# Performance work log

Measured on AMD Instinct MI355X. Metric: run time of the kernel, lower is better.

The kernel has to match this reference:

```python
import jax, jax.numpy as jnp
import numpy as np

GROUPS = [1, 2, 2, 3]

def setup_inputs() -> dict:
    key = jax.random.key(0)
    ks = jax.random.split(key, 8)
    b, dim, h, w = 8, 256, 64, 64
    return {
        "x": jax.random.normal(ks[0], (b, dim, h, w), dtype=jnp.float32),
        "temperature": jnp.ones((4, 1, 1), dtype=jnp.float32),          # nn.Parameter(torch.ones(4,1,1))
        "w_qkv": jax.random.normal(ks[1], (3 * dim, dim)) * 0.02,        # Conv2d(dim,3dim,1,bias=False)
        "w_dw": jax.random.normal(ks[2], (3 * dim, 1, 3, 3)) * 0.1,      # depthwise 3x3, groups=3dim
        "w_proj": jax.random.normal(ks[3], (dim, dim)) * 0.02,           # Conv2d(dim,dim,1,bias=False)
        "w_gate": jax.random.normal(ks[4], (dim, dim)) * 0.02,           # Intra gatingConv (Conv1d k=1)
        "b_gate": jnp.zeros((dim,), dtype=jnp.float32),
        "w_down": jax.random.normal(ks[5], (dim // 2, dim)) * 0.02,      # Intra down
        "b_down": jnp.zeros((dim // 2,), dtype=jnp.float32),
        "w_up": jax.random.normal(ks[6], (dim, dim // 2)) * 0.02,        # Intra up
        "b_up": jnp.zeros((dim,), dtype=jnp.float32),
    }

def _l2norm(t):
    # torch F.normalize(dim=-1): x / max(||x||, 1e-12)
    return t / jnp.maximum(jnp.linalg.norm(t, axis=-1, keepdims=True), 1e-12)

def reference(x, temperature, w_qkv, w_dw, w_proj, w_gate, b_gate, w_down, b_down, w_up, b_up):
    b, c, h, w = x.shape
    L = h * w
    # qkv = dwconv3x3(conv1x1(x))
    qkv = jnp.einsum('bchw,oc->bohw', x, w_qkv)
    qkv = jax.lax.conv_general_dilated(qkv, w_dw, (1, 1), ((1, 1), (1, 1)),
                                       feature_group_count=3 * c,
                                       dimension_numbers=('NCHW', 'OIHW', 'NCHW'))
    q, k, v = jnp.split(qkv, 3, axis=1)
    q = q.reshape(b, c, L); k = k.reshape(b, c, L); v = v.reshape(b, c, L)
    # ReGroup: sort channels by mean activation (descending), split per ratio
    order = jnp.argsort(-q.mean(axis=2).mean(axis=0))
    qs, ks_, vs = q[:, order], k[:, order], v[:, order]
    total = sum(GROUPS)
    sizes = [int(r / total * c) for r in GROUPS]
    sizes[-1] += c - sum(sizes)
    outs, caches = [], []
    start = 0
    for i, g in enumerate(sizes):
        qg = qs[:, start:start + g]; kg = ks_[:, start:start + g]; vg = vs[:, start:start + g]
        start += g
        qn = _l2norm(qg); kn = _l2norm(kg)
        attn = jax.nn.softmax(jnp.einsum('bcl,bdl->bcd', qn, kn) * temperature[i], axis=-1)  # (b,Cg,Cg)
        caches.append(jax.lax.stop_gradient(qn + kn))  # q.detach()+k.detach()
        outs.append(jnp.einsum('bcd,bdl->bcl', attn, vg))
    # CalculateCurrentLayerCache: mean over L, channel-tile to c, bilinear 1x1->sxs == broadcast
    s = int(L ** 0.5 + 0.9999)
    accum = jnp.zeros((b, c), dtype=x.dtype)
    for tc, g in zip(caches, sizes):
        gm = tc.mean(axis=-1)                     # (b, Cg)
        rep = max(1, c // g)
        tiled = jnp.tile(gm, (1, rep))
        if tiled.shape[1] > c:
            tiled = tiled[:, :c]
        elif tiled.shape[1] < c:
            tiled = jnp.pad(tiled, ((0, 0), (0, c - tiled.shape[1])))
        accum = accum + tiled
    accum = accum / len(caches)
    qv_cache = 0.9 * jnp.broadcast_to(accum[:, :, None, None], (b, c, s, s))
    out_all = jnp.concatenate(outs, axis=1)       # (b, c, L)
    tmp_caches = jnp.concatenate(caches, axis=1)  # (b, c, L)
    # Intra_CacheModulation: gated = gelu(gateConv(z)) * z ; out = up(down(gated))
    z = tmp_caches + out_all
    gating = jax.nn.gelu(jnp.einsum('oc,bcl->bol', w_gate, z) + b_gate[None, :, None], approximate=False)
    gated = gating * z
    mid = jnp.einsum('oc,bcl->bol', w_down, gated) + b_down[None, :, None]
    intra = jnp.einsum('oc,bcl->bol', w_up, mid) + b_up[None, :, None]
    out_all = (intra + out_all).reshape(b, c, h, w)
    out_all = jnp.einsum('bchw,oc->bohw', out_all, w_proj)
    return (out_all, qv_cache)
```

## Files before the change

kernel.cpp:

```cpp
#include <hip/hip_runtime.h>
#include <hip/hip_fp16.h>
#include <math.h>

#define B 8
#define C 256
#define L 4096
#define OC3 768

typedef __attribute__((ext_vector_type(8))) short short8v;
typedef __attribute__((ext_vector_type(8))) unsigned short u16x8;
typedef __attribute__((ext_vector_type(4))) float f32x4;

__device__ __forceinline__ float gelu_exact(float x){
  return 0.5f * x * (1.0f + erff(x * 0.70710678118654752440f));
}
__device__ __forceinline__ float wave_sum(float v){
  #pragma unroll
  for (int off = 32; off > 0; off >>= 1) v += __shfl_down(v, off, 64);
  return v;
}
__device__ __forceinline__ unsigned short f16b(float f){
  return __half_as_ushort(__float2half_rn(f));
}
__device__ __forceinline__ float f16tof(unsigned short u){
  return __half2float(__ushort_as_half(u));
}
__device__ __forceinline__ unsigned int splitpackh(float v){
  unsigned short hi = f16b(v);
  float lof = v - f16tof(hi);
  unsigned short lo = f16b(lof);
  return (unsigned int)hi | ((unsigned int)lo << 16);
}
__device__ __forceinline__ void gl16(const unsigned short* g, unsigned short* l){
  __builtin_amdgcn_global_load_lds(
      (const __attribute__((address_space(1))) void*)g,
      (__attribute__((address_space(3))) void*)l, 16, 0, 0);
}

__global__ __launch_bounds__(256) void wsplit_kernel(
    const float* __restrict__ wqkv, const float* __restrict__ wgate,
    const float* __restrict__ wdown, const float* __restrict__ wup,
    const float* __restrict__ wproj,
    unsigned short* __restrict__ Wf16,
    unsigned short* __restrict__ PH, unsigned short* __restrict__ PLo)
{
  int idx = blockIdx.x * 256 + threadIdx.x;
  if (idx < 327680) {
    float s;
    if (idx < 196608)      s = wqkv[idx];
    else if (idx < 262144) s = wgate[idx - 196608];
    else if (idx < 294912) s = wdown[idx - 262144];
    else                   s = wup[idx - 294912];
    Wf16[idx] = f16b(s);
  } else {
    int j = idx - 327680;
    float wv = wproj[j];
    unsigned short hh = f16b(wv);
    PH[j]  = hh;
    PLo[j] = f16b(wv - f16tof(hh));
  }
}

__global__ __launch_bounds__(256) void splitx_kernel(const float* __restrict__ x,
    unsigned short* __restrict__ XThi, unsigned short* __restrict__ XTlo)
{
  __shared__ float st[64][68];
  const int b = blockIdx.z, c0 = blockIdx.y * 64, lb = blockIdx.x * 64;
  const int t = threadIdx.x;
  #pragma unroll
  for (int i = 0; i < 4; i++) {
    int row = (t >> 4) + i * 16;
    int col = (t & 15) * 4;
    float4 v = *(const float4*)&x[((size_t)b * C + c0 + row) * L + lb + col];
    st[row][col] = v.x; st[row][col+1] = v.y; st[row][col+2] = v.z; st[row][col+3] = v.w;
  }
  __syncthreads();
  const int l = t >> 2, cq = t & 3;
  u16x8 hv0, hv1, lv0, lv1;
  #pragma unroll
  for (int i = 0; i < 16; i++) {
    unsigned int p = splitpackh(st[cq * 16 + i][l]);
    if (i < 8) { hv0[i] = (unsigned short)(p & 0xFFFFu); lv0[i] = (unsigned short)(p >> 16); }
    else       { hv1[i-8] = (unsigned short)(p & 0xFFFFu); lv1[i-8] = (unsigned short)(p >> 16); }
  }
  size_t o = ((size_t)b * L + lb + l) * C + c0 + cq * 16;
  *(u16x8*)&XThi[o]     = hv0;
  *(u16x8*)&XThi[o + 8] = hv1;
  *(u16x8*)&XTlo[o]     = lv0;
  *(u16x8*)&XTlo[o + 8] = lv1;
}

template<int KTOT, int EPI, int MODE>
__global__ __launch_bounds__(256) void hgemm(
    const unsigned short* __restrict__ Ahi_g, const unsigned short* __restrict__ Alo_g,
    const unsigned short* __restrict__ Bw_g,
    float* __restrict__ outF,
    unsigned short* __restrict__ outH,
    int Ntot)
{
  __shared__ unsigned short SB[2][3][128 * 32];
  const int t  = threadIdx.x;
  const int lb = blockIdx.x * 128;
  const int o0 = blockIdx.y * 128;
  const int b  = blockIdx.z;
  const int w  = t >> 6, lane = t & 63;
  const int wm = w >> 1, wn = w & 1;
  const int ln = lane & 15, lg = lane >> 4;
  const int lrow  = lane >> 2;
  const int chunk = (lane & 3) ^ ((lane >> 4) & 3);
  const int slot  = lg ^ (ln >> 2);
  const bool twop = (blockIdx.y < 2);

  f32x4 z4 = {0.f, 0.f, 0.f, 0.f};
  f32x4 acc[4][4];
  #pragma unroll
  for (int i = 0; i < 4; i++)
    #pragma unroll
    for (int j = 0; j < 4; j++) acc[i][j] = z4;

  const size_t arow0 = (size_t)b * L + lb;
  constexpr int NKT = KTOT / 32;

  auto stage = [&](int kt, int cb) {
    const int k0 = kt * 32;
    #pragma unroll
    for (int i = 0; i < 2; i++) {
      const int rb = w * 32 + i * 16;
      const size_t ga = (arow0 + rb + lrow) * KTOT + k0 + chunk * 8;
      gl16(Ahi_g + ga, &SB[cb][0][rb * 32]);
      if (twop) gl16(Alo_g + ga, &SB[cb][1][rb * 32]);
      const size_t gb = (size_t)(o0 + rb + lrow) * KTOT + k0 + chunk * 8;
      gl16(Bw_g + gb, &SB[cb][2][rb * 32]);
    }
  };

  stage(0, 0);
  __syncthreads();
  int cur = 0;
  for (int kt = 0; kt < NKT; ++kt) {
    if (kt + 1 < NKT) stage(kt + 1, cur ^ 1);
    short8v bwf[4];
    #pragma unroll
    for (int nf = 0; nf < 4; nf++) {
      const int off = (wn * 64 + nf * 16 + ln) * 32 + slot * 8;
      bwf[nf] = *(const short8v*)&SB[cur][2][off];
    }
    #pragma unroll
    for (int mf = 0; mf < 4; mf++) {
      const int off = (wm * 64 + mf * 16 + ln) * 32 + slot * 8;
      const short8v ah = *(const short8v*)&SB[cur][0][off];
      #pragma unroll
      for (int nf = 0; nf < 4; nf++)
        acc[mf][nf] = __builtin_amdgcn_mfma_f32_16x16x32_f16(ah, bwf[nf], acc[mf][nf], 0, 0, 0);
      if (twop) {
        const short8v al = *(const short8v*)&SB[cur][1][off];
        #pragma unroll
        for (int nf = 0; nf < 4; nf++)
          acc[mf][nf] = __builtin_amdgcn_mfma_f32_16x16x32_f16(al, bwf[nf], acc[mf][nf], 0, 0, 0);
      }
    }
    __syncthreads();
    cur ^= 1;
  }
  #pragma unroll
  for (int mf = 0; mf < 4; mf++) {
    const int mbase = lb + wm * 64 + mf * 16 + lg * 4;
    #pragma unroll
    for (int nf = 0; nf < 4; nf++) {
      const int o = o0 + wn * 64 + nf * 16 + ln;
      if (o0 < 256) {
        float4 r;
        r.x = acc[mf][nf][0]; r.y = acc[mf][nf][1];
        r.z = acc[mf][nf][2]; r.w = acc[mf][nf][3];
        *(float4*)&outF[((size_t)b * 256 + o) * L + mbase] = r;
      } else {
        ushort4 r;
        r.x = f16b(acc[mf][nf][0]); r.y = f16b(acc[mf][nf][1]);
        r.z = f16b(acc[mf][nf][2]); r.w = f16b(acc[mf][nf][3]);
        *(ushort4*)&outH[((size_t)b * 512 + (o - 256)) * L + mbase] = r;
      }
    }
  }
}

__global__ __launch_bounds__(256) void mlp_fused_kernel(
    const unsigned short* __restrict__ zT,
    const unsigned short* __restrict__ outT,
    const unsigned short* __restrict__ Wg,
    const unsigned short* __restrict__ Wd,
    const unsigned short* __restrict__ Wu,
    const unsigned short* __restrict__ WpH,
    const unsigned short* __restrict__ WpL,
    const float* __restrict__ bg, const float* __restrict__ bd, const float* __restrict__ bu,
    float* __restrict__ out0)
{
  __shared__ unsigned short zL[128 * 256];
  __shared__ unsigned short wL[128 * 128];
  __shared__ unsigned short mL[128 * 128];
  const int t = threadIdx.x;
  const int l0 = blockIdx.x * 128;
  const int b  = blockIdx.y;
  const int w = t >> 6, lane = t & 63;
  const int wm = w >> 1, wn = w & 1;
  const int ln = lane & 15, lg = lane >> 4;

  {
    const int rIn = lane >> 5, ch = lane & 31;
    #pragma unroll
    for (int j = 0; j < 16; j++) {
      const int rowbase = (j * 4 + w) * 2;
      const int row = rowbase + rIn;
      const int sc = ch ^ (row & 7);
      gl16(zT + ((size_t)b * L + l0 + row) * 256 + sc * 8, &zL[rowbase * 256]);
    }
  }

  auto stageW = [&](const unsigned short* src, int rowstride) {
    __syncthreads();
    const int rIn = lane >> 4, ch = lane & 15;
    #pragma unroll
    for (int j = 0; j < 8; j++) {
      const int rowbase = (j * 4 + w) * 4;
      const int row = rowbase + rIn;
      const int sc = ch ^ (row & 7);
      gl16(src + (size_t)row * rowstride + sc * 8, &wL[rowbase * 128]);
    }
    __syncthreads();
  };

  auto fragZ = [&](int row, int cc) -> short8v {
    return *(const short8v*)&zL[row * 256 + (cc ^ (row & 7)) * 8];
  };
  auto fragW = [&](int row, int cc) -> short8v {
    return *(const short8v*)&wL[row * 128 + (cc ^ (row & 7)) * 8];
  };
  auto fragM = [&](int row, int cc) -> short8v {
    return *(const short8v*)&mL[row * 128 + (cc ^ (row & 7)) * 8];
  };

  auto gemmZ = [&](f32x4 (&acc)[4][4], int cb) {
    #pragma unroll
    for (int ks = 0; ks < 4; ks++) {
      short8v bf[4];
      #pragma unroll
      for (int nf = 0; nf < 4; nf++)
        bf[nf] = fragW(wn * 64 + nf * 16 + ln, ks * 4 + lg);
      #pragma unroll
      for (int mf = 0; mf < 4; mf++) {
        const short8v af = fragZ(wm * 64 + mf * 16 + ln, cb + ks * 4 + lg);
        #pragma unroll
        for (int nf = 0; nf < 4; nf++)
          acc[mf][nf] = __builtin_amdgcn_mfma_f32_16x16x32_f16(af, bf[nf], acc[mf][nf], 0, 0, 0);
      }
    }
  };
  auto gemmM = [&](f32x4 (&acc)[4][4]) {
    #pragma unroll
    for (int ks = 0; ks < 4; ks++) {
      short8v bf[4];
      #pragma unroll
      for (int nf = 0; nf < 4; nf++)
        bf[nf] = fragW(wn * 64 + nf * 16 + ln, ks * 4 + lg);
      #pragma unroll
      for (int mf = 0; mf < 4; mf++) {
        const short8v af = fragM(wm * 64 + mf * 16 + ln, ks * 4 + lg);
        #pragma unroll
        for (int nf = 0; nf < 4; nf++)
          acc[mf][nf] = __builtin_amdgcn_mfma_f32_16x16x32_f16(af, bf[nf], acc[mf][nf], 0, 0, 0);
      }
    }
  };

  const f32x4 zz = {0.f, 0.f, 0.f, 0.f};

  f32x4 accG[2][4][4];
  #pragma unroll
  for (int nh = 0; nh < 2; nh++)
    #pragma unroll
    for (int i = 0; i < 4; i++)
      #pragma unroll
      for (int j = 0; j < 4; j++) accG[nh][i][j] = zz;
  for (int nh = 0; nh < 2; nh++)
    for (int kh = 0; kh < 2; kh++) {
      stageW(Wg + (size_t)(nh * 128) * 256 + kh * 128, 256);
      gemmZ(accG[nh], kh * 16);
    }
  __syncthreads();
  #pragma unroll
  for (int nh = 0; nh < 2; nh++)
    #pragma unroll
    for (int mf = 0; mf < 4; mf++)
      #pragma unroll
      for (int nf = 0; nf < 4; nf++)
        #pragma unroll
        for (int r = 0; r < 4; r++) {
          const int l = wm * 64 + mf * 16 + lg * 4 + r;
          const int o = nh * 128 + wn * 64 + nf * 16 + ln;
          const int a = l * 256 + (((o >> 3) ^ (l & 7)) << 3) + (o & 7);
          const float g = gelu_exact(accG[nh][mf][nf][r] + bg[o]) * f16tof(zL[a]);
          zL[a] = f16b(g);
        }
  f32x4 accD[4][4];
  #pragma unroll
  for (int i = 0; i < 4; i++)
    #pragma unroll
    for (int j = 0; j < 4; j++) accD[i][j] = zz;
  for (int kh = 0; kh < 2; kh++) {
    stageW(Wd + kh * 128, 256);
    gemmZ(accD, kh * 16);
  }
  __syncthreads();
  #pragma unroll
  for (int mf = 0; mf < 4; mf++)
    #pragma unroll
    for (int nf = 0; nf < 4; nf++)
      #pragma unroll
      for (int r = 0; r < 4; r++) {
        const int l = wm * 64 + mf * 16 + lg * 4 + r;
        const int o = wn * 64 + nf * 16 + ln;
        mL[l * 128 + (((o >> 3) ^ (l & 7)) << 3) + (o & 7)] = f16b(accD[mf][nf][r] + bd[o]);
      }
  for (int nh = 0; nh < 2; nh++) {
    f32x4 accU[4][4];
    #pragma unroll
    for (int i = 0; i < 4; i++)
      #pragma unroll
      for (int j = 0; j < 4; j++) accU[i][j] = zz;
    stageW(Wu + (size_t)(nh * 128) * 128, 128);
    gemmM(accU);
    #pragma unroll
    for (int mf = 0; mf < 4; mf++)
      #pragma unroll
      for (int nf = 0; nf < 4; nf++)
        #pragma unroll
        for (int r = 0; r < 4; r++) {
          const int l = wm * 64 + mf * 16 + lg * 4 + r;
          const int o = nh * 128 + wn * 64 + nf * 16 + ln;
          const float v = accU[mf][nf][r] + bu[o]
                        + f16tof(outT[((size_t)b * L + l0 + l) * 256 + o]);
          zL[l * 256 + (((o >> 3) ^ (l & 7)) << 3) + (o & 7)] = f16b(v);
        }
  }
  for (int nh = 0; nh < 2; nh++) {
    f32x4 accP[4][4];
    #pragma unroll
    for (int i = 0; i < 4; i++)
      #pragma unroll
      for (int j = 0; j < 4; j++) accP[i][j] = zz;
    for (int kh = 0; kh < 2; kh++) {
      stageW(WpH + (size_t)(nh * 128) * 256 + kh * 128, 256);
      gemmZ(accP, kh * 16);
      stageW(WpL + (size_t)(nh * 128) * 256 + kh * 128, 256);
      gemmZ(accP, kh * 16);
    }
    #pragma unroll
    for (int mf = 0; mf < 4; mf++) {
      const int mbase = l0 + wm * 64 + mf * 16 + lg * 4;
      #pragma unroll
      for (int nf = 0; nf < 4; nf++) {
        const int o = nh * 128 + wn * 64 + nf * 16 + ln;
        float4 r4;
        r4.x = accP[mf][nf][0]; r4.y = accP[mf][nf][1];
        r4.z = accP[mf][nf][2]; r4.w = accP[mf][nf][3];
        *(float4*)&out0[((size_t)b * 256 + o) * L + mbase] = r4;
      }
    }
  }
}

__global__ __launch_bounds__(256) void dwconv2_kernel(
    const float* __restrict__ inQ, const unsigned short* __restrict__ inKV,
    const float* __restrict__ wdw,
    unsigned short* __restrict__ qkF, unsigned short* __restrict__ vF,
    float* __restrict__ csum, float* __restrict__ csumsq)
{
  __shared__ float p[66][73];
  __shared__ float rs[4][2];
  const int ch = blockIdx.x;
  const int b  = blockIdx.y;
  const int t  = threadIdx.x;
  float wt[9];
  #pragma unroll
  for (int j = 0; j < 9; j++) wt[j] = wdw[ch * 9 + j];
  if (t < 66) { p[0][3 + t] = 0.f; p[65][3 + t] = 0.f; }
  if (t < 64) { p[1 + t][3] = 0.f; p[1 + t][68] = 0.f; }
  if (ch < 256) {
    const size_t base = ((size_t)b * 256 + ch) * L;
    #pragma unroll
    for (int i = 0; i < 4; i++) {
      int pix = (i * 256 + t) * 4;
      const float4 v = *reinterpret_cast<const float4*>(&inQ[base + pix]);
      int h = pix >> 6, ww = pix & 63;
      p[1+h][4+ww] = v.x; p[1+h][5+ww] = v.y; p[1+h][6+ww] = v.z; p[1+h][7+ww] = v.w;
    }
  } else {
    const size_t base = ((size_t)b * 512 + (ch - 256)) * L + t * 16;
    const u16x8 a0 = *(const u16x8*)&inKV[base];
    const u16x8 a1 = *(const u16x8*)&inKV[base + 8];
    const int h = t >> 2, w0 = (t & 3) * 16;
    #pragma unroll
    for (int j = 0; j < 8; j++) {
      p[1+h][4+w0+j]   = f16tof((unsigned short)a0[j]);
      p[1+h][12+w0+j]  = f16tof((unsigned short)a1[j]);
    }
  }
  __syncthreads();
  const int h  = t >> 2;
  const int w0 = (t & 3) * 16;
  float r0a[18], r1a[18], r2a[18];
  #pragma unroll
  for (int c = 0; c < 18; c++) {
    r0a[c] = p[h][w0 + 3 + c];
    r1a[c] = p[h + 1][w0 + 3 + c];
    r2a[c] = p[h + 2][w0 + 3 + c];
  }
  float res[16];
  float s = 0.f, s2 = 0.f;
  #pragma unroll
  for (int j = 0; j < 16; j++) {
    float acc;
    acc = r0a[j] * wt[0];
    acc = fmaf(r0a[j+1], wt[1], acc);
    acc = fmaf(r0a[j+2], wt[2], acc);
    acc = fmaf(r1a[j],   wt[3], acc);
    acc = fmaf(r1a[j+1], wt[4], acc);
    acc = fmaf(r1a[j+2], wt[5], acc);
    acc = fmaf(r2a[j],   wt[6], acc);
    acc = fmaf(r2a[j+1], wt[7], acc);
    acc = fmaf(r2a[j+2], wt[8], acc);
    res[j] = acc;
    s += acc;
    s2 = fmaf(acc, acc, s2);
  }
  u16x8 h0v, h1v;
  #pragma unroll
  for (int j = 0; j < 16; j++) {
    if (j < 8) h0v[j]   = f16b(res[j]);
    else       h1v[j-8] = f16b(res[j]);
  }
  if (ch < 512) {
    const size_t qi = ((size_t)b * 512 + ch) * L + t * 16;
    *(u16x8*)&qkF[qi]     = h0v;
    *(u16x8*)&qkF[qi + 8] = h1v;
    s = wave_sum(s); s2 = wave_sum(s2);
    const int lane = t & 63, wid = t >> 6;
    if (lane == 0) { rs[wid][0] = s; rs[wid][1] = s2; }
    __syncthreads();
    if (t == 0) {
      csum[b * 512 + ch]   = rs[0][0] + rs[1][0] + rs[2][0] + rs[3][0];
      csumsq[b * 512 + ch] = rs[0][1] + rs[1][1] + rs[2][1] + rs[3][1];
    }
  } else {
    const size_t vi = ((size_t)b * 256 + (ch - 512)) * L + t * 16;
    *(u16x8*)&vF[vi]     = h0v;
    *(u16x8*)&vF[vi + 8] = h1v;
  }
}

__global__ __launch_bounds__(256) void rankstats_kernel(
    const float* __restrict__ csum, const float* __restrict__ csumsq,
    int* __restrict__ order,
    float* __restrict__ sumq, float* __restrict__ sumk,
    float* __restrict__ invnq, float* __restrict__ invnk)
{
  const int c = threadIdx.x;
  float key = 0.f;
  #pragma unroll
  for (int b = 0; b < 8; b++) key += csum[b * 512 + c];
  __shared__ float keys[256];
  __shared__ int ordS[256];
  keys[c] = key;
  __syncthreads();
  int rank = 0;
  for (int j = 0; j < 256; j++) {
    float kj = keys[j];
    rank += (kj > key) || (kj == key && j < c);
  }
  order[rank] = c;
  ordS[rank] = c;
  __syncthreads();
  const int ch = ordS[c];
  #pragma unroll
  for (int b = 0; b < 8; b++) {
    sumq[b * 256 + c]  = csum[b * 512 + ch];
    invnq[b * 256 + c] = 1.0f / fmaxf(sqrtf(csumsq[b * 512 + ch]), 1e-12f);
    sumk[b * 256 + c]  = csum[b * 512 + 256 + ch];
    invnk[b * 256 + c] = 1.0f / fmaxf(sqrtf(csumsq[b * 512 + 256 + ch]), 1e-12f);
  }
}

__global__ __launch_bounds__(256) void vpack_kernel(
    const unsigned short* __restrict__ vF, const unsigned short* __restrict__ qkF,
    const int* __restrict__ order,
    const float* __restrict__ invnq, const float* __restrict__ invnk,
    unsigned short* __restrict__ vTS, unsigned short* __restrict__ zqT)
{
  __shared__ float vt[64][65];
  __shared__ float zt[64][65];
  __shared__ int   ordS[256];
  __shared__ float iqS[256], ikS[256];
  const int t = threadIdx.x, lb = blockIdx.x * 64, b = blockIdx.y;
  ordS[t] = order[t];
  iqS[t] = invnq[b * 256 + t];
  ikS[t] = invnk[b * 256 + t];
  __syncthreads();
  for (int cc = 0; cc < 4; cc++) {
    const int r0 = cc * 64;
    for (int i = t; i < 1024; i += 256) {
      const int row = i >> 4, q = i & 15;
      const int ch = ordS[r0 + row];
      const float iq = iqS[r0 + row], ik = ikS[r0 + row];
      const ushort4 v4 = *(const ushort4*)&vF[((size_t)b * 256 + ch) * L + lb + q * 4];
      vt[q*4+0][row] = f16tof(v4.x); vt[q*4+1][row] = f16tof(v4.y);
      vt[q*4+2][row] = f16tof(v4.z); vt[q*4+3][row] = f16tof(v4.w);
      const ushort4 q4 = *(const ushort4*)&qkF[((size_t)b * 512 + ch) * L + lb + q * 4];
      const ushort4 k4 = *(const ushort4*)&qkF[((size_t)b * 512 + 256 + ch) * L + lb + q * 4];
      zt[q*4+0][row] = f16tof(q4.x) * iq + f16tof(k4.x) * ik;
      zt[q*4+1][row] = f16tof(q4.y) * iq + f16tof(k4.y) * ik;
      zt[q*4+2][row] = f16tof(q4.z) * iq + f16tof(k4.z) * ik;
      zt[q*4+3][row] = f16tof(q4.w) * iq + f16tof(k4.w) * ik;
    }
    __syncthreads();
    const int l = t >> 2, qq = t & 3;
    const size_t ob = ((size_t)b * L + lb + l) * 256 + r0 + qq * 16;
    u16x8 vv[2], zz[2];
    #pragma unroll
    for (int j = 0; j < 16; j++) {
      vv[j>>3][j&7] = f16b(vt[l][qq*16 + j]);
      zz[j>>3][j&7] = f16b(zt[l][qq*16 + j]);
    }
    *(u16x8*)&vTS[ob]     = vv[0]; *(u16x8*)&vTS[ob + 8] = vv[1];
    *(u16x8*)&zqT[ob]     = zz[0]; *(u16x8*)&zqT[ob + 8] = zz[1];
    __syncthreads();
  }
}

template<int G, int GI, int START, int MB, int SPB>
__device__ void scores_body(const unsigned short* __restrict__ qkF,
    const int* __restrict__ order, float* __restrict__ Spart,
    unsigned short* Ah, unsigned short* Bh, int* ordS)
{
  constexpr int MR = (G - MB * 64 < 64) ? (G - MB * 64) : 64;
  constexpr int NF = G / 16;
  const int t = threadIdx.x, ks = blockIdx.x, b = blockIdx.y;
  const int w = t >> 6, lane = t & 63, ln = lane & 15, lg = lane >> 4;
  const int lrow  = lane >> 2;
  const int chunk = (lane & 3) ^ ((lane >> 4) & 3);
  const int slot  = lg ^ (ln >> 2);
  for (int i = t; i < G; i += 256) ordS[i] = order[START + i];
  __syncthreads();
  const int k0 = ks * 512;
  const bool act = (w * 16) < MR;
  f32x4 z4 = {0.f, 0.f, 0.f, 0.f};
  f32x4 acc[NF];
  #pragma unroll
  for (int i = 0; i < NF; i++) acc[i] = z4;

  auto stage = [&](int kc, int cb) {
    for (int i = w; i < MR / 16; i += 4) {
      const int rb = i * 16;
      const int ch = ordS[MB * 64 + rb + lrow];
      const size_t g = ((size_t)b * 512 + ch) * L + k0 + kc + chunk * 8;
      gl16(qkF + g, &Ah[cb * 2048 + rb * 32]);
    }
    for (int i = w; i < G / 16; i += 4) {
      const int rb = i * 16;
      const int ch = 256 + ordS[rb + lrow];
      const size_t g = ((size_t)b * 512 + ch) * L + k0 + kc + chunk * 8;
      gl16(qkF + g, &Bh[cb * 3072 + rb * 32]);
    }
  };

  stage(0, 0);
  __syncthreads();
  int cur = 0;
  for (int kc = 0; kc < 512; kc += 32) {
    if (kc + 32 < 512) stage(kc + 32, cur ^ 1);
    if (act) {
      const int aoff = cur * 2048 + (w * 16 + ln) * 32 + slot * 8;
      const short8v ah = *(const short8v*)&Ah[aoff];
      #pragma unroll
      for (int nf = 0; nf < NF; nf++) {
        const int boff = cur * 3072 + (nf * 16 + ln) * 32 + slot * 8;
        const short8v bh = *(const short8v*)&Bh[boff];
        acc[nf] = __builtin_amdgcn_mfma_f32_16x16x32_f16(ah, bh, acc[nf], 0, 0, 0);
      }
    }
    __syncthreads();
    cur ^= 1;
  }
  if (act) {
    float* dst = Spart + (size_t)b * 147456 + SPB + ks * G * G;
    #pragma unroll
    for (int nf = 0; nf < NF; nf++) {
      const int d = nf * 16 + ln;
      #pragma unroll
      for (int r = 0; r < 4; r++) {
        const int m = MB * 64 + w * 16 + lg * 4 + r;
        dst[m * G + d] = acc[nf][r];
      }
    }
  }
}

__global__ __launch_bounds__(256) void scores_kernel(const unsigned short* __restrict__ qkF,
    const int* __restrict__ order, float* __restrict__ Spart)
{
  __shared__ unsigned short Ah[2 * 64 * 32];
  __shared__ unsigned short Bh[2 * 96 * 32];
  __shared__ int ordS[96];
  switch (blockIdx.z) {
    case 0:  scores_body<32, 0, 0,   0, 0    >(qkF, order, Spart, Ah, Bh, ordS); break;
    case 1:  scores_body<64, 1, 32,  0, 8192 >(qkF, order, Spart, Ah, Bh, ordS); break;
    case 2:  scores_body<64, 2, 96,  0, 40960>(qkF, order, Spart, Ah, Bh, ordS); break;
    case 3:  scores_body<96, 3, 160, 0, 73728>(qkF, order, Spart, Ah, Bh, ordS); break;
    default: scores_body<96, 3, 160, 1, 73728>(qkF, order, Spart, Ah, Bh, ordS); break;
  }
}

template<int G, int GI, int START, int SPB, int AOFF>
__device__ void softmax_body(const float* __restrict__ Spart, const float* __restrict__ invnq,
    const float* __restrict__ invnk, const float* __restrict__ temperature,
    unsigned short* __restrict__ attnP, float* Sm)
{
  constexpr int RQ = G / 4;
  const int t = threadIdx.x;
  const int b = blockIdx.x;
  const int r0 = blockIdx.z * RQ;
  const float temp = temperature[GI];
  for (int idx = t; idx < RQ * G; idx += 256) {
    const int rl = idx / G, d = idx - rl * G;
    const int gidx = (r0 + rl) * G + d;
    float s = 0.f;
    #pragma unroll
    for (int ks = 0; ks < 8; ks++)
      s += Spart[(size_t)b * 147456 + SPB + ks * G * G + gidx];
    Sm[idx] = s * invnq[b * 256 + START + r0 + rl] * invnk[b * 256 + START + d] * temp;
  }
  __syncthreads();
  const int wv = t >> 6, lane = t & 63;
  for (int r = wv; r < RQ; r += 4) {
    const float v0 = (lane < G) ? Sm[r * G + lane] : -INFINITY;
    const float v1 = (64 + lane < G) ? Sm[r * G + 64 + lane] : -INFINITY;
    float m = fmaxf(v0, v1);
    #pragma unroll
    for (int off = 32; off > 0; off >>= 1) m = fmaxf(m, __shfl_xor(m, off, 64));
    const float e0 = (lane < G) ? expf(v0 - m) : 0.f;
    const float e1 = (64 + lane < G) ? expf(v1 - m) : 0.f;
    float s = e0 + e1;
    #pragma unroll
    for (int off = 32; off > 0; off >>= 1) s += __shfl_xor(s, off, 64);
    const float inv = 1.0f / s;
    const size_t base = (size_t)b * 18432 + AOFF + (size_t)(r0 + r) * G;
    if (lane < G)      attnP[base + lane]      = f16b(e0 * inv);
    if (64 + lane < G) attnP[base + 64 + lane] = f16b(e1 * inv);
  }
}

__global__ __launch_bounds__(256) void softmax_kernel(const float* __restrict__ Spart,
    const float* __restrict__ invnq, const float* __restrict__ invnk,
    const float* __restrict__ temperature, unsigned short* __restrict__ attnP)
{
  extern __shared__ float smem[];
  switch (blockIdx.y) {
    case 0:  softmax_body<32, 0, 0,   0,     0   >(Spart, invnq, invnk, temperature, attnP, smem); break;
    case 1:  softmax_body<64, 1, 32,  8192,  1024>(Spart, invnq, invnk, temperature, attnP, smem); break;
    case 2:  softmax_body<64, 2, 96,  40960, 5120>(Spart, invnq, invnk, temperature, attnP, smem); break;
    default: softmax_body<96, 3, 160, 73728, 9216>(Spart, invnq, invnk, temperature, attnP, smem); break;
  }
}

template<int G, int GI, int START, int AOFF>
__device__ void pv_body(
    const unsigned short* __restrict__ vTS, const unsigned short* __restrict__ attnP,
    const unsigned short* __restrict__ zqT,
    unsigned short* __restrict__ outT, unsigned short* __restrict__ zT,
    unsigned short* Ah, unsigned short* Bh)
{
  constexpr int NF = G / 16;
  const int t = threadIdx.x, b = blockIdx.y, l0 = blockIdx.x * 128;
  const int w = t >> 6, lane = t & 63, ln = lane & 15, lg = lane >> 4;
  const int lrow  = lane >> 2;
  const int chunk = (lane & 3) ^ ((lane >> 4) & 3);
  const int slot  = lg ^ (ln >> 2);
  f32x4 z4 = {0.f, 0.f, 0.f, 0.f};
  f32x4 acc[2][NF];
  #pragma unroll
  for (int i = 0; i < 2; i++)
    #pragma unroll
    for (int j = 0; j < NF; j++) acc[i][j] = z4;
  for (int kc = 0; kc < G; kc += 32) {
    #pragma unroll
    for (int i = 0; i < 2; i++) {
      const int rb = w * 32 + i * 16;
      const size_t g = ((size_t)b * L + l0 + rb + lrow) * 256 + START + kc + chunk * 8;
      gl16(vTS + g, &Ah[rb * 32]);
    }
    for (int i = w; i < G / 16; i += 4) {
      const int rb = i * 16;
      const size_t g = (size_t)b * 18432 + AOFF + (size_t)(rb + lrow) * G + kc + chunk * 8;
      gl16(attnP + g, &Bh[rb * 32]);
    }
    __syncthreads();
    short8v bhf[NF];
    #pragma unroll
    for (int nf = 0; nf < NF; nf++)
      bhf[nf] = *(const short8v*)&Bh[(nf * 16 + ln) * 32 + slot * 8];
    #pragma unroll
    for (int mi = 0; mi < 2; mi++) {
      const int aoff = ((w * 2 + mi) * 16 + ln) * 32 + slot * 8;
      const short8v ah = *(const short8v*)&Ah[aoff];
      #pragma unroll
      for (int nf = 0; nf < NF; nf++)
        acc[mi][nf] = __builtin_amdgcn_mfma_f32_16x16x32_f16(ah, bhf[nf], acc[mi][nf], 0, 0, 0);
    }
    __syncthreads();
  }
  #pragma unroll
  for (int mi = 0; mi < 2; mi++) {
    const int lbase = l0 + (w * 2 + mi) * 16 + lg * 4;
    #pragma unroll
    for (int nf = 0; nf < NF; nf++) {
      const int col = START + nf * 16 + ln;
      #pragma unroll
      for (int r = 0; r < 4; r++) {
        const size_t idx = ((size_t)b * L + lbase + r) * 256 + col;
        const float v = acc[mi][nf][r];
        outT[idx] = f16b(v);
        zT[idx]   = f16b(v + f16tof(zqT[idx]));
      }
    }
  }
}

__global__ __launch_bounds__(256) void pv_kernel(
    const unsigned short* __restrict__ vTS, const unsigned short* __restrict__ attnP,
    const unsigned short* __restrict__ zqT,
    unsigned short* __restrict__ outT, unsigned short* __restrict__ zT)
{
  __shared__ unsigned short Ah[128 * 32];
  __shared__ unsigned short Bh[96 * 32];
  switch (blockIdx.z) {
    case 0:  pv_body<32, 0, 0,   0   >(vTS, attnP, zqT, outT, zT, Ah, Bh); break;
    case 1:  pv_body<64, 1, 32,  1024>(vTS, attnP, zqT, outT, zT, Ah, Bh); break;
    case 2:  pv_body<64, 2, 96,  5120>(vTS, attnP, zqT, outT, zT, Ah, Bh); break;
    default: pv_body<96, 3, 160, 9216>(vTS, attnP, zqT, outT, zT, Ah, Bh); break;
  }
}

__global__ __launch_bounds__(256) void qv_kernel(const float* __restrict__ sumq,
    const float* __restrict__ sumk, const float* __restrict__ invnq,
    const float* __restrict__ invnk, float* __restrict__ out2)
{
  const int b = blockIdx.x >> 8, r = blockIdx.x & 255;
  float val = 0.f;
  {
    const int idx = b * 256 + 0 + (r & 31);
    val += fmaf(sumq[idx], invnq[idx], sumk[idx] * invnk[idx]);
  }
  {
    const int idx = b * 256 + 32 + (r & 63);
    val += fmaf(sumq[idx], invnq[idx], sumk[idx] * invnk[idx]);
  }
  {
    const int idx = b * 256 + 96 + (r & 63);
    val += fmaf(sumq[idx], invnq[idx], sumk[idx] * invnk[idx]);
  }
  if (r < 192) {
    const int rm = (r < 96) ? r : r - 96;
    const int idx = b * 256 + 160 + rm;
    val += fmaf(sumq[idx], invnq[idx], sumk[idx] * invnk[idx]);
  }
  val *= (1.0f / 4096.f) * 0.25f * 0.9f;
  const float4 o = {val, val, val, val};
  float4* dst = reinterpret_cast<float4*>(out2 + ((size_t)b * C + r) * L);
  for (int i = threadIdx.x; i < 1024; i += 256) dst[i] = o;
}

extern "C" void kernel_launch(void* const* d_in, const int* in_sizes, int n_in,
                              void* d_out, int out_size, void* d_ws, size_t ws_size,
                              hipStream_t stream)
{
  const float* x           = (const float*)d_in[0];
  const float* temperature = (const float*)d_in[1];
  const float* w_qkv       = (const float*)d_in[2];
  const float* w_dw        = (const float*)d_in[3];
  const float* w_proj      = (const float*)d_in[4];
  const float* w_gate      = (const float*)d_in[5];
  const float* b_gate      = (const float*)d_in[6];
  const float* w_down      = (const float*)d_in[7];
  const float* b_down      = (const float*)d_in[8];
  const float* w_up        = (const float*)d_in[9];
  const float* b_up        = (const float*)d_in[10];

  if (ws_size < 202548224ULL) return;

  char* ws = (char*)d_ws;
  float*          qkvQ    = (float*)(ws);
  unsigned short* kvF     = (unsigned short*)(ws + 33554432);
  unsigned short* vTS     = (unsigned short*)(ws);
  unsigned short* zqT     = (unsigned short*)(ws + 16777216);
  float*          Spart   = (float*)(ws + 33554432);
  unsigned short* attnP   = (unsigned short*)(ws + 38797312);
  unsigned short* XThi    = (unsigned short*)(ws + 100663296);
  unsigned short* XTlo    = (unsigned short*)(ws + 117440512);
  unsigned short* qkF     = (unsigned short*)(ws + 100663296);
  unsigned short* vF      = (unsigned short*)(ws + 134217728);
  unsigned short* outT    = (unsigned short*)(ws + 150994944);
  unsigned short* zT      = (unsigned short*)(ws + 167772160);
  unsigned short* Wf16   = (unsigned short*)(ws + 201326592);
  unsigned short* WprojH = (unsigned short*)(ws + 201981952);
  unsigned short* WprojL = (unsigned short*)(ws + 202113024);
  float* csum   = (float*)(ws + 202244096);
  float* csumsq = (float*)(ws + 202260480);
  float* sumq   = (float*)(ws + 202276864);
  float* sumk   = (float*)(ws + 202285056);
  float* invnq  = (float*)(ws + 202293248);
  float* invnk  = (float*)(ws + 202301440);
  int*   order  = (int*)(ws + 202309632);

  float* out_all = (float*)d_out;
  float* qv_out  = out_all + (size_t)B * C * L;

  wsplit_kernel<<<1536, 256, 0, stream>>>(w_qkv, w_gate, w_down, w_up, w_proj,
                                          Wf16, WprojH, WprojL);
  splitx_kernel<<<dim3(64, 4, 8), 256, 0, stream>>>(x, XThi, XTlo);
  hgemm<256, 6, 2><<<dim3(32, 6, 8), 256, 0, stream>>>(
      XThi, XTlo, Wf16, qkvQ, kvF, 768);
  dwconv2_kernel<<<dim3(768, 8), 256, 0, stream>>>(qkvQ, kvF, w_dw, qkF, vF, csum, csumsq);
  rankstats_kernel<<<1, 256, 0, stream>>>(csum, csumsq, order, sumq, sumk, invnq, invnk);
  vpack_kernel<<<dim3(64, 8), 256, 0, stream>>>(vF, qkF, order, invnq, invnk, vTS, zqT);
  scores_kernel<<<dim3(8, 8, 5), 256, 0, stream>>>(qkF, order, Spart);
  softmax_kernel<<<dim3(8, 4, 4), 256, 9216, stream>>>(Spart, invnq, invnk, temperature, attnP);
  pv_kernel<<<dim3(32, 8, 4), 256, 0, stream>>>(vTS, attnP, zqT, outT, zT);
  mlp_fused_kernel<<<dim3(32, 8), 256, 0, stream>>>(
      zT, outT, Wf16 + 196608, Wf16 + 262144, Wf16 + 294912, WprojH, WprojL,
      b_gate, b_down, b_up, out_all);
  qv_kernel<<<2048, 256, 0, stream>>>(sumq, sumk, invnq, invnk, qv_out);
}
```

Measured before the change: 219.7 us.

## Double-buffer weight tiles in fused MLP kernel to overlap loads with MFMA

The fused gate/down/up/proj kernel now keeps two weight tiles in shared memory. It issues the global-to-LDS load of the next weight tile before running the MFMA GEMM on the current one, which replaces the old pattern of a sync, a load and another sync before every GEMM. The mid buffer now aliases the z tile so LDS use stays about the same (64KB+64KB), and the up GEMMs are done for both halves before they are written back into z. The risks are a hidden race from the aliasing or the sync placement, and higher register pressure from the double accumulator accU.

```diff
diff --git a/kernel.cpp b/kernel.cpp
--- a/kernel.cpp
+++ b/kernel.cpp
@@ -195,8 +195,8 @@
     float* __restrict__ out0)
 {
   __shared__ unsigned short zL[128 * 256];
-  __shared__ unsigned short wL[128 * 128];
-  __shared__ unsigned short mL[128 * 128];
+  __shared__ unsigned short wL[2][128 * 128];
+  unsigned short* mL = zL;
   const int t = threadIdx.x;
   const int l0 = blockIdx.x * 128;
   const int b  = blockIdx.y;
@@ -214,37 +214,34 @@
       gl16(zT + ((size_t)b * L + l0 + row) * 256 + sc * 8, &zL[rowbase * 256]);
     }
   }
-
-  auto stageW = [&](const unsigned short* src, int rowstride) {
-    __syncthreads();
+  auto issueW = [&](int cb, const unsigned short* src, int rowstride) {
     const int rIn = lane >> 4, ch = lane & 15;
     #pragma unroll
     for (int j = 0; j < 8; j++) {
       const int rowbase = (j * 4 + w) * 4;
       const int row = rowbase + rIn;
       const int sc = ch ^ (row & 7);
-      gl16(src + (size_t)row * rowstride + sc * 8, &wL[rowbase * 128]);
-    }
-    __syncthreads();
+      gl16(src + (size_t)row * rowstride + sc * 8, &wL[cb][rowbase * 128]);
+    }
   };
 
   auto fragZ = [&](int row, int cc) -> short8v {
     return *(const short8v*)&zL[row * 256 + (cc ^ (row & 7)) * 8];
   };
-  auto fragW = [&](int row, int cc) -> short8v {
-    return *(const short8v*)&wL[row * 128 + (cc ^ (row & 7)) * 8];
+  auto fragW = [&](int cb, int row, int cc) -> short8v {
+    return *(const short8v*)&wL[cb][row * 128 + (cc ^ (row & 7)) * 8];
   };
   auto fragM = [&](int row, int cc) -> short8v {
     return *(const short8v*)&mL[row * 128 + (cc ^ (row & 7)) * 8];
   };
 
-  auto gemmZ = [&](f32x4 (&acc)[4][4], int cb) {
+  auto gemmZ = [&](f32x4 (&acc)[4][4], int cb, int buf) {
     #pragma unroll
     for (int ks = 0; ks < 4; ks++) {
       short8v bf[4];
       #pragma unroll
       for (int nf = 0; nf < 4; nf++)
-        bf[nf] = fragW(wn * 64 + nf * 16 + ln, ks * 4 + lg);
+        bf[nf] = fragW(buf, wn * 64 + nf * 16 + ln, ks * 4 + lg);
       #pragma unroll
       for (int mf = 0; mf < 4; mf++) {
         const short8v af = fragZ(wm * 64 + mf * 16 + ln, cb + ks * 4 + lg);
@@ -254,13 +251,13 @@
       }
     }
   };
-  auto gemmM = [&](f32x4 (&acc)[4][4]) {
+  auto gemmM = [&](f32x4 (&acc)[4][4], int buf) {
     #pragma unroll
     for (int ks = 0; ks < 4; ks++) {
       short8v bf[4];
       #pragma unroll
       for (int nf = 0; nf < 4; nf++)
-        bf[nf] = fragW(wn * 64 + nf * 16 + ln, ks * 4 + lg);
+        bf[nf] = fragW(buf, wn * 64 + nf * 16 + ln, ks * 4 + lg);
       #pragma unroll
       for (int mf = 0; mf < 4; mf++) {
         const short8v af = fragM(wm * 64 + mf * 16 + ln, ks * 4 + lg);
@@ -272,6 +269,21 @@
   };
 
   const f32x4 zz = {0.f, 0.f, 0.f, 0.f};
+  const unsigned short* G00 = Wg;
+  const unsigned short* G01 = Wg + 128;
+  const unsigned short* G10 = Wg + 128 * 256;
+  const unsigned short* G11 = Wg + 128 * 256 + 128;
+  const unsigned short* D0  = Wd;
+  const unsigned short* D1  = Wd + 128;
+  const unsigned short* U0  = Wu;
+  const unsigned short* U1  = Wu + 128 * 128;
+  const unsigned short* PH00 = WpH,                  *PL00 = WpL;
+  const unsigned short* PH01 = WpH + 128,            *PL01 = WpL + 128;
+  const unsigned short* PH10 = WpH + 128 * 256,      *PL10 = WpL + 128 * 256;
+  const unsigned short* PH11 = WpH + 128 * 256 + 128,*PL11 = WpL + 128 * 256 + 128;
+
+  issueW(0, G00, 256);
+  __syncthreads();
 
   f32x4 accG[2][4][4];
   #pragma unroll
@@ -280,12 +292,10 @@
     for (int i = 0; i < 4; i++)
       #pragma unroll
       for (int j = 0; j < 4; j++) accG[nh][i][j] = zz;
-  for (int nh = 0; nh < 2; nh++)
-    for (int kh = 0; kh < 2; kh++) {
-      stageW(Wg + (size_t)(nh * 128) * 256 + kh * 128, 256);
-      gemmZ(accG[nh], kh * 16);
-    }
-  __syncthreads();
+  issueW(1, G01, 256); gemmZ(accG[0], 0,  0); __syncthreads();
+  issueW(0, G10, 256); gemmZ(accG[0], 16, 1); __syncthreads();
+  issueW(1, G11, 256); gemmZ(accG[1], 0,  0); __syncthreads();
+  issueW(0, D0,  256); gemmZ(accG[1], 16, 1); __syncthreads();
   #pragma unroll
   for (int nh = 0; nh < 2; nh++)
     #pragma unroll
@@ -300,16 +310,14 @@
           const float g = gelu_exact(accG[nh][mf][nf][r] + bg[o]) * f16tof(zL[a]);
           zL[a] = f16b(g);
         }
+  __syncthreads();
   f32x4 accD[4][4];
   #pragma unroll
   for (int i = 0; i < 4; i++)
     #pragma unroll
     for (int j = 0; j < 4; j++) accD[i][j] = zz;
-  for (int kh = 0; kh < 2; kh++) {
-    stageW(Wd + kh * 128, 256);
-    gemmZ(accD, kh * 16);
-  }
-  __syncthreads();
+  issueW(1, D1, 256); gemmZ(accD, 0,  0); __syncthreads();
+  issueW(0, U0, 128); gemmZ(accD, 16, 1); __syncthreads();
   #pragma unroll
   for (int mf = 0; mf < 4; mf++)
     #pragma unroll
@@ -320,14 +328,18 @@
         const int o = wn * 64 + nf * 16 + ln;
         mL[l * 128 + (((o >> 3) ^ (l & 7)) << 3) + (o & 7)] = f16b(accD[mf][nf][r] + bd[o]);
       }
-  for (int nh = 0; nh < 2; nh++) {
-    f32x4 accU[4][4];
+  __syncthreads();
+  f32x4 accU[2][4][4];
+  #pragma unroll
+  for (int nh = 0; nh < 2; nh++)
     #pragma unroll
     for (int i = 0; i < 4; i++)
       #pragma unroll
-      for (int j = 0; j < 4; j++) accU[i][j] = zz;
-    stageW(Wu + (size_t)(nh * 128) * 128, 128);
-    gemmM(accU);
+      for (int j = 0; j < 4; j++) accU[nh][i][j] = zz;
+  issueW(1, U1,   128); gemmM(accU[0], 0); __syncthreads();
+  issueW(0, PH00, 256); gemmM(accU[1], 1); __syncthreads();
+  #pragma unroll
+  for (int nh = 0; nh < 2; nh++)
     #pragma unroll
     for (int mf = 0; mf < 4; mf++)
       #pragma unroll
@@ -336,23 +348,12 @@
         for (int r = 0; r < 4; r++) {
           const int l = wm * 64 + mf * 16 + lg * 4 + r;
           const int o = nh * 128 + wn * 64 + nf * 16 + ln;
-          const float v = accU[mf][nf][r] + bu[o]
+          const float v = accU[nh][mf][nf][r] + bu[o]
                         + f16tof(outT[((size_t)b * L + l0 + l) * 256 + o]);
           zL[l * 256 + (((o >> 3) ^ (l & 7)) << 3) + (o & 7)] = f16b(v);
         }
-  }
-  for (int nh = 0; nh < 2; nh++) {
-    f32x4 accP[4][4];
-    #pragma unroll
-    for (int i = 0; i < 4; i++)
-      #pragma unroll
-      for (int j = 0; j < 4; j++) accP[i][j] = zz;
-    for (int kh = 0; kh < 2; kh++) {
-      stageW(WpH + (size_t)(nh * 128) * 256 + kh * 128, 256);
-      gemmZ(accP, kh * 16);
-      stageW(WpL + (size_t)(nh * 128) * 256 + kh * 128, 256);
-      gemmZ(accP, kh * 16);
-    }
+  __syncthreads();
+  auto projWrite = [&](f32x4 (&accP)[4][4], int nh) {
     #pragma unroll
     for (int mf = 0; mf < 4; mf++) {
       const int mbase = l0 + wm * 64 + mf * 16 + lg * 4;
@@ -365,7 +366,26 @@
         *(float4*)&out0[((size_t)b * 256 + o) * L + mbase] = r4;
       }
     }
-  }
+  };
+  f32x4 accP[4][4];
+  #pragma unroll
+  for (int i = 0; i < 4; i++)
+    #pragma unroll
+    for (int j = 0; j < 4; j++) accP[i][j] = zz;
+  issueW(1, PL00, 256); gemmZ(accP, 0,  0); __syncthreads();
+  issueW(0, PH01, 256); gemmZ(accP, 0,  1); __syncthreads();
+  issueW(1, PL01, 256); gemmZ(accP, 16, 0); __syncthreads();
+  issueW(0, PH10, 256); gemmZ(accP, 16, 1); __syncthreads();
+  projWrite(accP, 0);
+  #pragma unroll
+  for (int i = 0; i < 4; i++)
+    #pragma unroll
+    for (int j = 0; j < 4; j++) accP[i][j] = zz;
+  issueW(1, PL10, 256); gemmZ(accP, 0,  0); __syncthreads();
+  issueW(0, PH11, 256); gemmZ(accP, 0,  1); __syncthreads();
+  issueW(1, PL11, 256); gemmZ(accP, 16, 0); __syncthreads();
+  gemmZ(accP, 16, 1);
+  projWrite(accP, 1);
 }
 
 __global__ __launch_bounds__(256) void dwconv2_kernel(
```

Measured after the change: 222.5 us. Within noise of the previous version (+1.3%).

## Halve MLP tile rows and double-buffer weight staging with prefetch

Applied to the files above, without the earlier changes.

The fused MLP kernel now processes 64 sequence rows per block instead of 128, which doubles the grid to 512 blocks and raises occupancy via launch_bounds(256,2). Weight tiles are staged into two LDS buffers, so the next 64x128 tile loads while the current one is consumed by MFMA, and one barrier per step replaces two. Each wave now owns 16 rows across all output columns. In exchange, every weight is streamed twice as often from global/L2 and each MFMA step reuses fewer A-fragments.

```diff
diff --git a/kernel.cpp b/kernel.cpp
--- a/kernel.cpp
+++ b/kernel.cpp
@@ -183,7 +183,7 @@
   }
 }
 
-__global__ __launch_bounds__(256) void mlp_fused_kernel(
+__global__ __launch_bounds__(256, 2) void mlp_fused_kernel(
     const unsigned short* __restrict__ zT,
     const unsigned short* __restrict__ outT,
     const unsigned short* __restrict__ Wg,
@@ -194,178 +194,166 @@
     const float* __restrict__ bg, const float* __restrict__ bd, const float* __restrict__ bu,
     float* __restrict__ out0)
 {
-  __shared__ unsigned short zL[128 * 256];
-  __shared__ unsigned short wL[128 * 128];
-  __shared__ unsigned short mL[128 * 128];
+  __shared__ unsigned short zL[64 * 256];
+  __shared__ unsigned short wL[2][64 * 128];
+  __shared__ unsigned short mL[64 * 128];
   const int t = threadIdx.x;
-  const int l0 = blockIdx.x * 128;
+  const int l0 = blockIdx.x * 64;
   const int b  = blockIdx.y;
   const int w = t >> 6, lane = t & 63;
-  const int wm = w >> 1, wn = w & 1;
   const int ln = lane & 15, lg = lane >> 4;
 
   {
     const int rIn = lane >> 5, ch = lane & 31;
     #pragma unroll
-    for (int j = 0; j < 16; j++) {
-      const int rowbase = (j * 4 + w) * 2;
+    for (int j = 0; j < 8; j++) {
+      const int rowbase = w * 16 + j * 2;
       const int row = rowbase + rIn;
       const int sc = ch ^ (row & 7);
       gl16(zT + ((size_t)b * L + l0 + row) * 256 + sc * 8, &zL[rowbase * 256]);
     }
   }
-
-  auto stageW = [&](const unsigned short* src, int rowstride) {
-    __syncthreads();
+  auto issueW = [&](int cb, const unsigned short* src, int rowstride) {
     const int rIn = lane >> 4, ch = lane & 15;
     #pragma unroll
-    for (int j = 0; j < 8; j++) {
-      const int rowbase = (j * 4 + w) * 4;
+    for (int j = 0; j < 4; j++) {
+      const int rowbase = j * 16 + w * 4;
       const int row = rowbase + rIn;
       const int sc = ch ^ (row & 7);
-      gl16(src + (size_t)row * rowstride + sc * 8, &wL[rowbase * 128]);
-    }
-    __syncthreads();
+      gl16(src + (size_t)row * rowstride + sc * 8, &wL[cb][rowbase * 128]);
+    }
   };
-
   auto fragZ = [&](int row, int cc) -> short8v {
     return *(const short8v*)&zL[row * 256 + (cc ^ (row & 7)) * 8];
   };
-  auto fragW = [&](int row, int cc) -> short8v {
-    return *(const short8v*)&wL[row * 128 + (cc ^ (row & 7)) * 8];
+  auto fragW = [&](int cb, int row, int cc) -> short8v {
+    return *(const short8v*)&wL[cb][row * 128 + (cc ^ (row & 7)) * 8];
   };
   auto fragM = [&](int row, int cc) -> short8v {
     return *(const short8v*)&mL[row * 128 + (cc ^ (row & 7)) * 8];
   };
-
-  auto gemmZ = [&](f32x4 (&acc)[4][4], int cb) {
+  auto gemmZt = [&](f32x4 (&acc)[4], int buf, int cbase) {
     #pragma unroll
     for (int ks = 0; ks < 4; ks++) {
-      short8v bf[4];
-      #pragma unroll
-      for (int nf = 0; nf < 4; nf++)
-        bf[nf] = fragW(wn * 64 + nf * 16 + ln, ks * 4 + lg);
-      #pragma unroll
-      for (int mf = 0; mf < 4; mf++) {
-        const short8v af = fragZ(wm * 64 + mf * 16 + ln, cb + ks * 4 + lg);
-        #pragma unroll
-        for (int nf = 0; nf < 4; nf++)
-          acc[mf][nf] = __builtin_amdgcn_mfma_f32_16x16x32_f16(af, bf[nf], acc[mf][nf], 0, 0, 0);
+      const short8v af = fragZ(w * 16 + ln, cbase + ks * 4 + lg);
+      #pragma unroll
+      for (int nf = 0; nf < 4; nf++) {
+        const short8v bf = fragW(buf, nf * 16 + ln, ks * 4 + lg);
+        acc[nf] = __builtin_amdgcn_mfma_f32_16x16x32_f16(af, bf, acc[nf], 0, 0, 0);
       }
     }
   };
-  auto gemmM = [&](f32x4 (&acc)[4][4]) {
+  auto gemmMt = [&](f32x4 (&acc)[4], int buf) {
     #pragma unroll
     for (int ks = 0; ks < 4; ks++) {
-      short8v bf[4];
-      #pragma unroll
-      for (int nf = 0; nf < 4; nf++)
-        bf[nf] = fragW(wn * 64 + nf * 16 + ln, ks * 4 + lg);
-      #pragma unroll
-      for (int mf = 0; mf < 4; mf++) {
-        const short8v af = fragM(wm * 64 + mf * 16 + ln, ks * 4 + lg);
-        #pragma unroll
-        for (int nf = 0; nf < 4; nf++)
-          acc[mf][nf] = __builtin_amdgcn_mfma_f32_16x16x32_f16(af, bf[nf], acc[mf][nf], 0, 0, 0);
+      const short8v af = fragM(w * 16 + ln, ks * 4 + lg);
+      #pragma unroll
+      for (int nf = 0; nf < 4; nf++) {
+        const short8v bf = fragW(buf, nf * 16 + ln, ks * 4 + lg);
+        acc[nf] = __builtin_amdgcn_mfma_f32_16x16x32_f16(af, bf, acc[nf], 0, 0, 0);
       }
     }
   };
 
   const f32x4 zz = {0.f, 0.f, 0.f, 0.f};
-
-  f32x4 accG[2][4][4];
-  #pragma unroll
-  for (int nh = 0; nh < 2; nh++)
-    #pragma unroll
-    for (int i = 0; i < 4; i++)
-      #pragma unroll
-      for (int j = 0; j < 4; j++) accG[nh][i][j] = zz;
-  for (int nh = 0; nh < 2; nh++)
-    for (int kh = 0; kh < 2; kh++) {
-      stageW(Wg + (size_t)(nh * 128) * 256 + kh * 128, 256);
-      gemmZ(accG[nh], kh * 16);
-    }
-  __syncthreads();
-  #pragma unroll
-  for (int nh = 0; nh < 2; nh++)
-    #pragma unroll
-    for (int mf = 0; mf < 4; mf++)
-      #pragma unroll
-      for (int nf = 0; nf < 4; nf++)
-        #pragma unroll
-        for (int r = 0; r < 4; r++) {
-          const int l = wm * 64 + mf * 16 + lg * 4 + r;
-          const int o = nh * 128 + wn * 64 + nf * 16 + ln;
-          const int a = l * 256 + (((o >> 3) ^ (l & 7)) << 3) + (o & 7);
-          const float g = gelu_exact(accG[nh][mf][nf][r] + bg[o]) * f16tof(zL[a]);
-          zL[a] = f16b(g);
-        }
-  f32x4 accD[4][4];
+  issueW(0, Wg, 256);
+  __syncthreads();
+
+  f32x4 aG[4][4];
   #pragma unroll
   for (int i = 0; i < 4; i++)
     #pragma unroll
-    for (int j = 0; j < 4; j++) accD[i][j] = zz;
-  for (int kh = 0; kh < 2; kh++) {
-    stageW(Wd + kh * 128, 256);
-    gemmZ(accD, kh * 16);
-  }
-  __syncthreads();
-  #pragma unroll
-  for (int mf = 0; mf < 4; mf++)
+    for (int j = 0; j < 4; j++) aG[i][j] = zz;
+  issueW(1, Wg + 128,           256); gemmZt(aG[0], 0, 0);  __syncthreads();
+  issueW(0, Wg + 64*256,        256); gemmZt(aG[0], 1, 16); __syncthreads();
+  issueW(1, Wg + 64*256 + 128,  256); gemmZt(aG[1], 0, 0);  __syncthreads();
+  issueW(0, Wg + 128*256,       256); gemmZt(aG[1], 1, 16); __syncthreads();
+  issueW(1, Wg + 128*256 + 128, 256); gemmZt(aG[2], 0, 0);  __syncthreads();
+  issueW(0, Wg + 192*256,       256); gemmZt(aG[2], 1, 16); __syncthreads();
+  issueW(1, Wg + 192*256 + 128, 256); gemmZt(aG[3], 0, 0);  __syncthreads();
+  issueW(0, Wd,                 256); gemmZt(aG[3], 1, 16); __syncthreads();
+  #pragma unroll
+  for (int oc = 0; oc < 4; oc++)
     #pragma unroll
     for (int nf = 0; nf < 4; nf++)
       #pragma unroll
       for (int r = 0; r < 4; r++) {
-        const int l = wm * 64 + mf * 16 + lg * 4 + r;
-        const int o = wn * 64 + nf * 16 + ln;
-        mL[l * 128 + (((o >> 3) ^ (l & 7)) << 3) + (o & 7)] = f16b(accD[mf][nf][r] + bd[o]);
-      }
-  for (int nh = 0; nh < 2; nh++) {
-    f32x4 accU[4][4];
-    #pragma unroll
-    for (int i = 0; i < 4; i++)
-      #pragma unroll
-      for (int j = 0; j < 4; j++) accU[i][j] = zz;
-    stageW(Wu + (size_t)(nh * 128) * 128, 128);
-    gemmM(accU);
-    #pragma unroll
-    for (int mf = 0; mf < 4; mf++)
-      #pragma unroll
-      for (int nf = 0; nf < 4; nf++)
-        #pragma unroll
-        for (int r = 0; r < 4; r++) {
-          const int l = wm * 64 + mf * 16 + lg * 4 + r;
-          const int o = nh * 128 + wn * 64 + nf * 16 + ln;
-          const float v = accU[mf][nf][r] + bu[o]
-                        + f16tof(outT[((size_t)b * L + l0 + l) * 256 + o]);
-          zL[l * 256 + (((o >> 3) ^ (l & 7)) << 3) + (o & 7)] = f16b(v);
-        }
-  }
-  for (int nh = 0; nh < 2; nh++) {
-    f32x4 accP[4][4];
-    #pragma unroll
-    for (int i = 0; i < 4; i++)
-      #pragma unroll
-      for (int j = 0; j < 4; j++) accP[i][j] = zz;
-    for (int kh = 0; kh < 2; kh++) {
-      stageW(WpH + (size_t)(nh * 128) * 256 + kh * 128, 256);
-      gemmZ(accP, kh * 16);
-      stageW(WpL + (size_t)(nh * 128) * 256 + kh * 128, 256);
-      gemmZ(accP, kh * 16);
-    }
-    #pragma unroll
-    for (int mf = 0; mf < 4; mf++) {
-      const int mbase = l0 + wm * 64 + mf * 16 + lg * 4;
-      #pragma unroll
-      for (int nf = 0; nf < 4; nf++) {
-        const int o = nh * 128 + wn * 64 + nf * 16 + ln;
-        float4 r4;
-        r4.x = accP[mf][nf][0]; r4.y = accP[mf][nf][1];
-        r4.z = accP[mf][nf][2]; r4.w = accP[mf][nf][3];
-        *(float4*)&out0[((size_t)b * 256 + o) * L + mbase] = r4;
-      }
-    }
-  }
+        const int l = w * 16 + lg * 4 + r;
+        const int o = oc * 64 + nf * 16 + ln;
+        const int a = l * 256 + (((o >> 3) ^ (l & 7)) << 3) + (o & 7);
+        zL[a] = f16b(gelu_exact(aG[oc][nf][r] + bg[o]) * f16tof(zL[a]));
+      }
+  f32x4 aD[2][4];
+  #pragma unroll
+  for (int i = 0; i < 2; i++)
+    #pragma unroll
+    for (int j = 0; j < 4; j++) aD[i][j] = zz;
+  issueW(1, Wd + 128,           256); gemmZt(aD[0], 0, 0);  __syncthreads();
+  issueW(0, Wd + 64*256,        256); gemmZt(aD[0], 1, 16); __syncthreads();
+  issueW(1, Wd + 64*256 + 128,  256); gemmZt(aD[1], 0, 0);  __syncthreads();
+  issueW(0, Wu,                 128); gemmZt(aD[1], 1, 16); __syncthreads();
+  #pragma unroll
+  for (int oc = 0; oc < 2; oc++)
+    #pragma unroll
+    for (int nf = 0; nf < 4; nf++)
+      #pragma unroll
+      for (int r = 0; r < 4; r++) {
+        const int l = w * 16 + lg * 4 + r;
+        const int o = oc * 64 + nf * 16 + ln;
+        mL[l * 128 + (((o >> 3) ^ (l & 7)) << 3) + (o & 7)] = f16b(aD[oc][nf][r] + bd[o]);
+      }
+  f32x4 aU[4][4];
+  #pragma unroll
+  for (int i = 0; i < 4; i++)
+    #pragma unroll
+    for (int j = 0; j < 4; j++) aU[i][j] = zz;
+  issueW(1, Wu + 64*128,        128); gemmMt(aU[0], 0); __syncthreads();
+  issueW(0, Wu + 128*128,       128); gemmMt(aU[1], 1); __syncthreads();
+  issueW(1, Wu + 192*128,       128); gemmMt(aU[2], 0); __syncthreads();
+  issueW(0, WpH,                256); gemmMt(aU[3], 1); __syncthreads();
+  #pragma unroll
+  for (int oc = 0; oc < 4; oc++)
+    #pragma unroll
+    for (int nf = 0; nf < 4; nf++)
+      #pragma unroll
+      for (int r = 0; r < 4; r++) {
+        const int l = w * 16 + lg * 4 + r;
+        const int o = oc * 64 + nf * 16 + ln;
+        const float v = aU[oc][nf][r] + bu[o]
+                      + f16tof(outT[((size_t)b * L + l0 + l) * 256 + o]);
+        zL[l * 256 + (((o >> 3) ^ (l & 7)) << 3) + (o & 7)] = f16b(v);
+      }
+  f32x4 aP[4][4];
+  #pragma unroll
+  for (int i = 0; i < 4; i++)
+    #pragma unroll
+    for (int j = 0; j < 4; j++) aP[i][j] = zz;
+  issueW(1, WpL,                256); gemmZt(aP[0], 0, 0);  __syncthreads();
+  issueW(0, WpH + 128,          256); gemmZt(aP[0], 1, 0);  __syncthreads();
+  issueW(1, WpL + 128,          256); gemmZt(aP[0], 0, 16); __syncthreads();
+  issueW(0, WpH + 64*256,       256); gemmZt(aP[0], 1, 16); __syncthreads();
+  issueW(1, WpL + 64*256,       256); gemmZt(aP[1], 0, 0);  __syncthreads();
+  issueW(0, WpH + 64*256 + 128, 256); gemmZt(aP[1], 1, 0);  __syncthreads();
+  issueW(1, WpL + 64*256 + 128, 256); gemmZt(aP[1], 0, 16); __syncthreads();
+  issueW(0, WpH + 128*256,      256); gemmZt(aP[1], 1, 16); __syncthreads();
+  issueW(1, WpL + 128*256,      256); gemmZt(aP[2], 0, 0);  __syncthreads();
+  issueW(0, WpH + 128*256 + 128,256); gemmZt(aP[2], 1, 0);  __syncthreads();
+  issueW(1, WpL + 128*256 + 128,256); gemmZt(aP[2], 0, 16); __syncthreads();
+  issueW(0, WpH + 192*256,      256); gemmZt(aP[2], 1, 16); __syncthreads();
+  issueW(1, WpL + 192*256,      256); gemmZt(aP[3], 0, 0);  __syncthreads();
+  issueW(0, WpH + 192*256 + 128,256); gemmZt(aP[3], 1, 0);  __syncthreads();
+  issueW(1, WpL + 192*256 + 128,256); gemmZt(aP[3], 0, 16); __syncthreads();
+                                      gemmZt(aP[3], 1, 16);
+  #pragma unroll
+  for (int oc = 0; oc < 4; oc++)
+    #pragma unroll
+    for (int nf = 0; nf < 4; nf++) {
+      const int o = oc * 64 + nf * 16 + ln;
+      float4 r4;
+      r4.x = aP[oc][nf][0]; r4.y = aP[oc][nf][1];
+      r4.z = aP[oc][nf][2]; r4.w = aP[oc][nf][3];
+      *(float4*)&out0[((size_t)b * 256 + o) * L + l0 + w * 16 + lg * 4] = r4;
+    }
 }
 
 __global__ __launch_bounds__(256) void dwconv2_kernel(
@@ -833,7 +821,7 @@
   scores_kernel<<<dim3(8, 8, 5), 256, 0, stream>>>(qkF, order, Spart);
   softmax_kernel<<<dim3(8, 4, 4), 256, 9216, stream>>>(Spart, invnq, invnk, temperature, attnP);
   pv_kernel<<<dim3(32, 8, 4), 256, 0, stream>>>(vTS, attnP, zqT, outT, zT);
-  mlp_fused_kernel<<<dim3(32, 8), 256, 0, stream>>>(
+  mlp_fused_kernel<<<dim3(64, 8), 256, 0, stream>>>(
       zT, outT, Wf16 + 196608, Wf16 + 262144, Wf16 + 294912, WprojH, WprojL,
       b_gate, b_down, b_up, out_all);
   qv_kernel<<<2048, 256, 0, stream>>>(sumq, sumk, invnq, invnk, qv_out);
```

Result: faster. 206.8 us, median of 2 (-5.9%).
